# Kernel tuning notes

Hardware: AMD Instinct MI355X
Metric: run time of the kernel (lower is better)

## Reference

```python
import jax, jax.numpy as jnp
import numpy as np

KH, KW, STRIDE = 5, 5, 1
OUT_CH = 64


def setup_inputs() -> dict:
    key = jax.random.key(0)
    k1, k2 = jax.random.split(key)
    x = jax.random.normal(k1, (16, 1, 256, 256), dtype=jnp.float32)
    # kaiming_uniform_(a=sqrt(5)) on fan_in=25 gives bound ~= sqrt(6/((1+5)*25)) ~= 0.2
    w = jax.random.uniform(k2, (OUT_CH, 1, KH, KW), dtype=jnp.float32, minval=-0.2, maxval=0.2)
    w = w.at[0].set(0.0)  # reset_parameters zeroes the first filter
    return {"x": x, "weight": w}


def reference(x, weight):
    """Faithful vectorized RBF_Conv2d forward.

    Original: for each output pixel (k,l), cdist between the flattened window
    (B, kh*kw) and flattened weights (O, kh*kw), std = sample std (ddof=1) of
    the (B,O) distance matrix, output = gauss(dist, std) = exp(-0.5*(d/std)^2).
    """
    B = x.shape[0]
    O = weight.shape[0]
    # im2col: (B, P=kh*kw, Ho, Wo), valid padding (in_channels == 1)
    patches = jax.lax.conv_general_dilated_patches(
        x, (KH, KW), (STRIDE, STRIDE), 'VALID')
    wf = weight.reshape(O, -1)                                  # (O, P)
    pn = jnp.sum(patches * patches, axis=1)                     # (B, Ho, Wo)
    wn = jnp.sum(wf * wf, axis=1)                               # (O,)
    cross = jnp.einsum('bphw,op->bohw', patches, wf)            # (B, O, Ho, Wo)
    d2 = pn[:, None] + wn[None, :, None, None] - 2.0 * cross
    dist = jnp.sqrt(jnp.maximum(d2, 1e-12))                     # euclidean cdist
    # per-output-pixel sample std (ddof=1) over the (B, O) distance matrix
    mean = jnp.mean(dist, axis=(0, 1), keepdims=True)           # (1,1,Ho,Wo)
    var = jnp.sum((dist - mean) ** 2, axis=(0, 1), keepdims=True) / (B * O - 1)
    std = jnp.sqrt(var)
    # gauss RBF
    return jnp.exp(-0.5 * (dist / std) ** 2)
```

## Files before the change

kernel.cpp:

```cpp
#include <hip/hip_runtime.h>

typedef float v2f __attribute__((ext_vector_type(2)));

#define KH 5
#define KW 5
#define HH 256
#define WW 256
#define HO 252
#define WO 252
#define NB 16
#define NO 64
#define TL 16
#define XC (TL + KW - 1)
#define PLANE (HO * WO)

__global__ __launch_bounds__(512, 4)
void rbf_conv2d_kernel(const float* __restrict__ x, const float* __restrict__ w,
                       float* __restrict__ out) {
    __shared__ float xs[NB][KH][XC];
    __shared__ float wn[NO];
    __shared__ float partial[32][TL];
    __shared__ float meanv[TL];
    __shared__ float cinv[TL];

    const int t  = threadIdx.x;
    const int k  = blockIdx.y;
    const int a0 = (4 * k) & 15;
    const int l0 = a0 - TL + (blockIdx.x << 4);
    if (l0 >= WO || l0 + TL <= 0) return;

    for (int idx = t; idx < NB * KH * XC; idx += 512) {
        int b   = idx / (KH * XC);
        int rem = idx % (KH * XC);
        int r   = rem / XC;
        int c   = rem % XC;
        int col = l0 + c;
        col = col < 0 ? 0 : (col > WW - 1 ? WW - 1 : col);
        xs[b][r][c] = x[(b * HH + k + r) * WW + col];
    }
    if (t < NO) {
        float s = 0.f;
        #pragma unroll
        for (int i = 0; i < 25; ++i) { float v = w[t * 25 + i]; s = fmaf(v, v, s); }
        wn[t] = s;
    }
    __syncthreads();

    const int p = t & 15;
    const int b = (t >> 4) & 15;
    const int obase = __builtin_amdgcn_readfirstlane((t >> 8) << 5);

    float pr[25];
    float pn = 0.f;
    #pragma unroll
    for (int r = 0; r < KH; ++r)
        #pragma unroll
        for (int c = 0; c < KW; ++c) {
            float v = xs[b][r][p + c];
            pr[r * KW + c] = v;
            pn = fmaf(v, v, pn);
        }
    v2f prv[12];
    #pragma unroll
    for (int i = 0; i < 12; ++i) { prv[i].x = pr[2 * i]; prv[i].y = pr[2 * i + 1]; }
    const float pr24 = pr[24];

    v2f dv[16];
    #pragma unroll
    for (int j = 0; j < 16; ++j) {
        float cr0, cr1;
        {
            const float* __restrict__ wr = w + (obase + 2 * j) * 25;
            v2f acc = {0.f, 0.f};
            #pragma unroll
            for (int i = 0; i < 12; ++i) {
                v2f wv; wv.x = wr[2 * i]; wv.y = wr[2 * i + 1];
                acc = __builtin_elementwise_fma(prv[i], wv, acc);
            }
            cr0 = acc.x + acc.y + pr24 * wr[24];
        }
        {
            const float* __restrict__ wr = w + (obase + 2 * j + 1) * 25;
            v2f acc = {0.f, 0.f};
            #pragma unroll
            for (int i = 0; i < 12; ++i) {
                v2f wv; wv.x = wr[2 * i]; wv.y = wr[2 * i + 1];
                acc = __builtin_elementwise_fma(prv[i], wv, acc);
            }
            cr1 = acc.x + acc.y + pr24 * wr[24];
        }
        float d20 = fmaxf(fmaf(-2.f, cr0, pn + wn[obase + 2 * j]),     1e-12f);
        float d21 = fmaxf(fmaf(-2.f, cr1, pn + wn[obase + 2 * j + 1]), 1e-12f);
        dv[j].x = __builtin_amdgcn_sqrtf(d20);
        dv[j].y = __builtin_amdgcn_sqrtf(d21);
    }

    {
        float s = 0.f;
        #pragma unroll
        for (int j = 0; j < 16; ++j) s += dv[j].x + dv[j].y;
        partial[t >> 4][p] = s;
    }
    __syncthreads();
    if (t < TL) {
        float m = 0.f;
        #pragma unroll
        for (int q = 0; q < 32; ++q) m += partial[q][t];
        meanv[t] = m * (1.0f / 1024.0f);
    }
    __syncthreads();
    {
        const float m = meanv[p];
        float vs = 0.f;
        #pragma unroll
        for (int j = 0; j < 16; ++j) {
            float d0 = dv[j].x - m, d1 = dv[j].y - m;
            vs = fmaf(d0, d0, fmaf(d1, d1, vs));
        }
        partial[t >> 4][p] = vs;
    }
    __syncthreads();
    if (t < TL) {
        float v = 0.f;
        #pragma unroll
        for (int q = 0; q < 32; ++q) v += partial[q][t];
        v *= (1.0f / 1023.0f);
        cinv[t] = -0.72134752044448170368f / v;
    }
    __syncthreads();

    {
        const int l = l0 + p;
        const bool ok = (l >= 0) && (l < WO);
        const float c = cinv[p];
        v2f cv; cv.x = c; cv.y = c;
        const int base = ((b * NO + obase) * HO + k) * WO + l;
        #pragma unroll
        for (int j = 0; j < 16; ++j) {
            v2f tt = dv[j] * dv[j];
            tt = tt * cv;
            float e0 = exp2f(tt.x);
            float e1 = exp2f(tt.y);
            if (ok) {
                out[base + (2 * j) * PLANE]     = e0;
                out[base + (2 * j + 1) * PLANE] = e1;
            }
        }
    }
}

extern "C" void kernel_launch(void* const* d_in, const int* in_sizes, int n_in,
                              void* d_out, int out_size, void* d_ws, size_t ws_size,
                              hipStream_t stream) {
    const float* x = (const float*)d_in[0];
    const float* w = (const float*)d_in[1];
    float* out = (float*)d_out;
    dim3 grid(17, HO);
    rbf_conv2d_kernel<<<grid, 512, 0, stream>>>(x, w, out);
}
```

Baseline: 319.2 us.

## Process five column passes per block with one-pass variance and shuffle reductions

Each block now covers an 80-column span (64-column stride) in five 16-column passes, instead of one 16-column tile per block. The grid shrinks from 17 to 6 blocks per row, so fewer blocks pay for the staging and weight-norm setup. Variance is computed in a single pass from the sums of distance and squared distance, using wave shuffles and fewer barriers. Neighbouring blocks recompute 16 overlapping columns and split the even and odd channel stores between them. The trade-offs are extra redundant arithmetic and possible precision loss from the E[x^2]-mean^2 variance form.

```diff
diff --git a/kernel.cpp b/kernel.cpp
--- a/kernel.cpp
+++ b/kernel.cpp
@@ -10,31 +10,31 @@
 #define WO 252
 #define NB 16
 #define NO 64
-#define TL 16
-#define XC (TL + KW - 1)
 #define PLANE (HO * WO)
+#define NPASS 5
+#define XC 85
 
 __global__ __launch_bounds__(512, 4)
 void rbf_conv2d_kernel(const float* __restrict__ x, const float* __restrict__ w,
                        float* __restrict__ out) {
     __shared__ float xs[NB][KH][XC];
     __shared__ float wn[NO];
-    __shared__ float partial[32][TL];
-    __shared__ float meanv[TL];
-    __shared__ float cinv[TL];
+    __shared__ float pS1[2][8][16];
+    __shared__ float pS2[2][8][16];
 
     const int t  = threadIdx.x;
     const int k  = blockIdx.y;
-    const int a0 = (4 * k) & 15;
-    const int l0 = a0 - TL + (blockIdx.x << 4);
-    if (l0 >= WO || l0 + TL <= 0) return;
+    const int a0 = (4 * k) & 31;
+    const int Le = a0 - 64 + 64 * (int)blockIdx.x;
+    if (Le - 16 >= WO || Le + 64 <= 0) return;
+    const int colbase = Le - 16;
 
     for (int idx = t; idx < NB * KH * XC; idx += 512) {
         int b   = idx / (KH * XC);
-        int rem = idx % (KH * XC);
+        int rem = idx - b * (KH * XC);
         int r   = rem / XC;
-        int c   = rem % XC;
-        int col = l0 + c;
+        int c   = rem - r * XC;
+        int col = colbase + c;
         col = col < 0 ? 0 : (col > WW - 1 ? WW - 1 : col);
         xs[b][r][c] = x[(b * HH + k + r) * WW + col];
     }
@@ -46,104 +46,96 @@
     }
     __syncthreads();
 
-    const int p = t & 15;
-    const int b = (t >> 4) & 15;
+    const int p     = t & 15;
+    const int b     = (t >> 4) & 15;
     const int obase = __builtin_amdgcn_readfirstlane((t >> 8) << 5);
+    const int wv    = t >> 6;
+    const int lane  = t & 63;
+    const int bo_base = ((b * NO + obase) * HO + k) * WO;
 
-    float pr[25];
-    float pn = 0.f;
-    #pragma unroll
-    for (int r = 0; r < KH; ++r)
-        #pragma unroll
-        for (int c = 0; c < KW; ++c) {
-            float v = xs[b][r][p + c];
-            pr[r * KW + c] = v;
-            pn = fmaf(v, v, pn);
+    #pragma unroll 1
+    for (int pi = 0; pi < NPASS; ++pi) {
+        const int  Lp     = colbase + 16 * pi;
+        const bool active = (Lp + 16 > 0) && (Lp < WO);
+        const int  pb     = pi & 1;
+
+        v2f   dv[16];
+        float s1 = 0.f, s2 = 0.f;
+
+        if (active) {
+            float pr[25];
+            float pn = 0.f;
+            #pragma unroll
+            for (int r = 0; r < KH; ++r)
+                #pragma unroll
+                for (int c = 0; c < KW; ++c) {
+                    float v = xs[b][r][16 * pi + p + c];
+                    pr[r * KW + c] = v;
+                    pn = fmaf(v, v, pn);
+                }
+            v2f prv[12];
+            #pragma unroll
+            for (int i = 0; i < 12; ++i) { prv[i].x = pr[2 * i]; prv[i].y = pr[2 * i + 1]; }
+            const float pr24 = pr[24];
+
+            #pragma unroll
+            for (int j = 0; j < 16; ++j) {
+                float cr0, cr1;
+                {
+                    const float* __restrict__ wr = w + (obase + 2 * j) * 25;
+                    v2f acc = {0.f, 0.f};
+                    #pragma unroll
+                    for (int i = 0; i < 12; ++i) {
+                        v2f wv_; wv_.x = wr[2 * i]; wv_.y = wr[2 * i + 1];
+                        acc = __builtin_elementwise_fma(prv[i], wv_, acc);
+                    }
+                    cr0 = acc.x + acc.y + pr24 * wr[24];
+                }
+                {
+                    const float* __restrict__ wr = w + (obase + 2 * j + 1) * 25;
+                    v2f acc = {0.f, 0.f};
+                    #pragma unroll
+                    for (int i = 0; i < 12; ++i) {
+                        v2f wv_; wv_.x = wr[2 * i]; wv_.y = wr[2 * i + 1];
+                        acc = __builtin_elementwise_fma(prv[i], wv_, acc);
+                    }
+                    cr1 = acc.x + acc.y + pr24 * wr[24];
+                }
+                float d20 = fmaxf(fmaf(-2.f, cr0, pn + wn[obase + 2 * j]),     1e-12f);
+                float d21 = fmaxf(fmaf(-2.f, cr1, pn + wn[obase + 2 * j + 1]), 1e-12f);
+                s2 += d20 + d21;
+                dv[j].x = __builtin_amdgcn_sqrtf(d20);
+                dv[j].y = __builtin_amdgcn_sqrtf(d21);
+                s1 += dv[j].x + dv[j].y;
+            }
+
+            s1 += __shfl_xor(s1, 16); s2 += __shfl_xor(s2, 16);
+            s1 += __shfl_xor(s1, 32); s2 += __shfl_xor(s2, 32);
+            if (lane < 16) { pS1[pb][wv][lane] = s1; pS2[pb][wv][lane] = s2; }
         }
-    v2f prv[12];
-    #pragma unroll
-    for (int i = 0; i < 12; ++i) { prv[i].x = pr[2 * i]; prv[i].y = pr[2 * i + 1]; }
-    const float pr24 = pr[24];
+        __syncthreads();
 
-    v2f dv[16];
-    #pragma unroll
-    for (int j = 0; j < 16; ++j) {
-        float cr0, cr1;
-        {
-            const float* __restrict__ wr = w + (obase + 2 * j) * 25;
-            v2f acc = {0.f, 0.f};
+        if (active) {
+            float S1 = 0.f, S2 = 0.f;
             #pragma unroll
-            for (int i = 0; i < 12; ++i) {
-                v2f wv; wv.x = wr[2 * i]; wv.y = wr[2 * i + 1];
-                acc = __builtin_elementwise_fma(prv[i], wv, acc);
-            }
-            cr0 = acc.x + acc.y + pr24 * wr[24];
-        }
-        {
-            const float* __restrict__ wr = w + (obase + 2 * j + 1) * 25;
-            v2f acc = {0.f, 0.f};
+            for (int q = 0; q < 8; ++q) { S1 += pS1[pb][q][p]; S2 += pS2[pb][q][p]; }
+            const float var  = (S2 - S1 * S1 * (1.0f / 1024.0f)) * (1.0f / 1023.0f);
+            const float cinv = -0.72134752044448170368f / var;
+
+            const int  l   = Lp + p;
+            const bool ok  = (l >= 0) && (l < WO);
+            const bool okE = ok && (pi >= 1);
+            const bool okO = ok && (pi <= 3);
+            v2f cv; cv.x = cinv; cv.y = cinv;
+            const int base = bo_base + l;
             #pragma unroll
-            for (int i = 0; i < 12; ++i) {
-                v2f wv; wv.x = wr[2 * i]; wv.y = wr[2 * i + 1];
-                acc = __builtin_elementwise_fma(prv[i], wv, acc);
-            }
-            cr1 = acc.x + acc.y + pr24 * wr[24];
-        }
-        float d20 = fmaxf(fmaf(-2.f, cr0, pn + wn[obase + 2 * j]),     1e-12f);
-        float d21 = fmaxf(fmaf(-2.f, cr1, pn + wn[obase + 2 * j + 1]), 1e-12f);
-        dv[j].x = __builtin_amdgcn_sqrtf(d20);
-        dv[j].y = __builtin_amdgcn_sqrtf(d21);
-    }
-
-    {
-        float s = 0.f;
-        #pragma unroll
-        for (int j = 0; j < 16; ++j) s += dv[j].x + dv[j].y;
-        partial[t >> 4][p] = s;
-    }
-    __syncthreads();
-    if (t < TL) {
-        float m = 0.f;
-        #pragma unroll
-        for (int q = 0; q < 32; ++q) m += partial[q][t];
-        meanv[t] = m * (1.0f / 1024.0f);
-    }
-    __syncthreads();
-    {
-        const float m = meanv[p];
-        float vs = 0.f;
-        #pragma unroll
-        for (int j = 0; j < 16; ++j) {
-            float d0 = dv[j].x - m, d1 = dv[j].y - m;
-            vs = fmaf(d0, d0, fmaf(d1, d1, vs));
-        }
-        partial[t >> 4][p] = vs;
-    }
-    __syncthreads();
-    if (t < TL) {
-        float v = 0.f;
-        #pragma unroll
-        for (int q = 0; q < 32; ++q) v += partial[q][t];
-        v *= (1.0f / 1023.0f);
-        cinv[t] = -0.72134752044448170368f / v;
-    }
-    __syncthreads();
-
-    {
-        const int l = l0 + p;
-        const bool ok = (l >= 0) && (l < WO);
-        const float c = cinv[p];
-        v2f cv; cv.x = c; cv.y = c;
-        const int base = ((b * NO + obase) * HO + k) * WO + l;
-        #pragma unroll
-        for (int j = 0; j < 16; ++j) {
-            v2f tt = dv[j] * dv[j];
-            tt = tt * cv;
-            float e0 = exp2f(tt.x);
-            float e1 = exp2f(tt.y);
-            if (ok) {
-                out[base + (2 * j) * PLANE]     = e0;
-                out[base + (2 * j + 1) * PLANE] = e1;
+            for (int j = 0; j < 16; ++j) {
+                v2f tt = dv[j] * dv[j];
+                tt = tt * cv;
+                float e0 = exp2f(tt.x);
+                float e1 = exp2f(tt.y);
+                if (okE) out[base + (2 * j) * PLANE]     = e0;
+                if (okO) out[base + (2 * j + 1) * PLANE] = e1;
             }
         }
     }
@@ -155,6 +147,6 @@
     const float* x = (const float*)d_in[0];
     const float* w = (const float*)d_in[1];
     float* out = (float*)d_out;
-    dim3 grid(17, HO);
+    dim3 grid(6, HO);
     rbf_conv2d_kernel<<<grid, 512, 0, stream>>>(x, w, out);
 }
```

Measured after the change: 349.5 us. +9.5%, slower.
